# Kernel optimization log

Measured on AMD Instinct MI355X. Metric: run time of the kernel, lower is better.

Reference implementation:

```python
import jax, jax.numpy as jnp
import numpy as np

D_MODEL, D_K, D_V = 1024, 64, 64
B, S = 4, 4096


def setup_inputs() -> dict:
    key = jax.random.key(0)
    ks = jax.random.split(key, 13)
    s = 1.0 / np.sqrt(D_MODEL)
    inp = {
        "q": jax.random.normal(ks[0], (B, S, D_MODEL), jnp.float32),
        "k": jax.random.normal(ks[1], (B, S, D_MODEL), jnp.float32),
        "v": jax.random.normal(ks[2], (B, S, D_MODEL), jnp.float32),
        "mask": jax.random.randint(ks[3], (1, S, S), 0, 2, jnp.int32),
        "Wq": jax.random.normal(ks[4], (D_K, D_MODEL), jnp.float32) * s,
        "bq": jax.random.normal(ks[5], (D_K,), jnp.float32) * s,
        "Wk": jax.random.normal(ks[6], (D_K, D_MODEL), jnp.float32) * s,
        "bk": jax.random.normal(ks[7], (D_K,), jnp.float32) * s,
        "Wv": jax.random.normal(ks[8], (D_V, D_MODEL), jnp.float32) * s,
        "bv": jax.random.normal(ks[9], (D_V,), jnp.float32) * s,
        "Wo": jax.random.normal(ks[10], (D_MODEL, D_V), jnp.float32) / np.sqrt(D_V),
        "bo": jax.random.normal(ks[11], (D_MODEL,), jnp.float32) / np.sqrt(D_V),
    }
    return inp


def reference(q, k, v, mask, Wq, bq, Wk, bk, Wv, bv, Wo, bo):
    # linear projections (torch Linear: x @ W.T + b)
    qh = jnp.einsum("bsd,kd->bsk", q, Wq) + bq   # [B,S,d_k]
    kh = jnp.einsum("bsd,kd->bsk", k, Wk) + bk   # [B,S,d_k]
    vh = jnp.einsum("bsd,vd->bsv", v, Wv) + bv   # [B,S,d_v]
    scale = 1.0 / jnp.sqrt(jnp.float32(D_K))
    scores = jnp.einsum("bqk,bmk->bqm", qh, kh) * scale  # [B,S,S]
    scores = jnp.where(mask == 0, jnp.float32(-1e9), scores)
    attn = jax.nn.softmax(scores, axis=-1)
    out = jnp.einsum("bqm,bmv->bqv", attn, vh)   # [B,S,d_v]
    return jnp.einsum("bqv,dv->bqd", out, Wo) + bo
```

## Files before the change

kernel.cpp:

```cpp
#include <hip/hip_runtime.h>
#include <cmath>

typedef __attribute__((ext_vector_type(8))) short bf16x8;
typedef __attribute__((ext_vector_type(4))) short bf16x4;
typedef __attribute__((ext_vector_type(4))) float f32x4;
typedef unsigned int u32;
typedef __attribute__((address_space(1))) const u32 gu32;
typedef __attribute__((address_space(3))) u32 lu32;

constexpr int B_ = 4;
constexpr int S_ = 4096;
constexpr int DM_ = 1024;
constexpr int DK_ = 64;
constexpr int NROW = B_ * S_;

__device__ __forceinline__ short f2bf(float x) {
  union { float f; unsigned u; } c; c.f = x;
  unsigned r = (c.u + 0x7FFF + ((c.u >> 16) & 1)) >> 16;
  return (short)r;
}
__device__ __forceinline__ float bf2f(short h) {
  union { float f; unsigned u; } c; c.u = ((unsigned)(unsigned short)h) << 16;
  return c.f;
}
__device__ __forceinline__ void gl16(const void* g, void* l) {
  __builtin_amdgcn_global_load_lds((gu32*)g, (lu32*)l, 16, 0, 0);
}

__global__ __launch_bounds__(256) void prep(
    const int* __restrict__ mask, unsigned long long* __restrict__ bits,
    const float* __restrict__ Wq, const float* __restrict__ Wk,
    const float* __restrict__ Wv, short* __restrict__ wbf) {
  if (blockIdx.x < 1024) {
    const int wid = (blockIdx.x * 256 + threadIdx.x) >> 6;
    const int lane = threadIdx.x & 63;
    const size_t base = (size_t)wid * 4096;
    for (int it = 0; it < 64; ++it) {
      int m = mask[base + it * 64 + lane];
      unsigned long long b = __ballot(m != 0);
      if (lane == 0) bits[(size_t)wid * 64 + it] = b;
    }
  } else {
    const int mat = blockIdx.x - 1024;
    const float* W = mat == 0 ? Wq : (mat == 1 ? Wk : Wv);
    short* dst = wbf + (size_t)mat * DK_ * DM_;
    const int t = threadIdx.x;
#pragma unroll 4
    for (int i = 0; i < 32; ++i) {
      int idx = i * 2048 + t * 8;
      f32x4 a0 = *(const f32x4*)(W + idx);
      f32x4 a1 = *(const f32x4*)(W + idx + 4);
      bf16x8 h;
#pragma unroll
      for (int j = 0; j < 4; ++j) { h[j] = f2bf(a0[j]); h[j + 4] = f2bf(a1[j]); }
      *(bf16x8*)(dst + idx) = h;
    }
  }
}

__global__ __launch_bounds__(256, 3) void proj_mfma(
    const float* __restrict__ q, const float* __restrict__ k,
    const float* __restrict__ v, const short* __restrict__ wbf,
    const float* __restrict__ bq, const float* __restrict__ bk,
    const float* __restrict__ bv,
    short* __restrict__ qh, short* __restrict__ kh, short* __restrict__ vhT) {
  __shared__ short wlds[2][64][64];

  const int mat = blockIdx.z;
  const float* X    = mat == 0 ? q : (mat == 1 ? k : v);
  const short* W    = wbf + (size_t)mat * DK_ * DM_;
  const float* bias = mat == 0 ? bq : (mat == 1 ? bk : bv);

  const int t = threadIdx.x;
  const int row0 = blockIdx.x * 64;
  const int lane = t & 63, w = t >> 6, quad = lane >> 4, l16 = lane & 15;

  const int myrow = row0 + 16 * w + l16;
  const float* xp = X + (size_t)myrow * DM_ + quad * 8;

  const int grA = 16 * w + (lane >> 3);
  const int scolh = (((lane & 7) ^ (lane >> 3)) * 8);
  const short* wsrcA = W + (size_t)grA * DM_ + scolh;
  const short* wsrcB = W + (size_t)(grA + 8) * DM_ + scolh;
  short* wdstA0 = &wlds[0][16 * w][0] + lane * 8;
  short* wdstB0 = &wlds[0][16 * w + 8][0] + lane * 8;
  short* wdstA1 = &wlds[1][16 * w][0] + lane * 8;
  short* wdstB1 = &wlds[1][16 * w + 8][0] + lane * 8;

  const int rsw = (l16 & 7) << 4;

  f32x4 acc[4] = {};
  f32x4 xr[4][4];

  gl16(wsrcA, wdstA0);
  gl16(wsrcB, wdstB0);
#pragma unroll
  for (int pb = 0; pb < 2; ++pb) {
    const float* s = xp + pb * 64;
    xr[pb][0] = *(const f32x4*)(s + 0);
    xr[pb][1] = *(const f32x4*)(s + 4);
    xr[pb][2] = *(const f32x4*)(s + 32);
    xr[pb][3] = *(const f32x4*)(s + 36);
  }
  asm volatile("s_waitcnt vmcnt(8)" ::: "memory");
  __builtin_amdgcn_s_barrier();
  __builtin_amdgcn_sched_barrier(0);

  auto compute_step = [&](int i, int buf) {
    const char* wb = (const char*)&wlds[buf][0][0];
    bf16x8 wf[2][4];
#pragma unroll
    for (int c = 0; c < 2; ++c)
#pragma unroll
      for (int ct = 0; ct < 4; ++ct)
        wf[c][ct] = *(const bf16x8*)(wb + (16 * ct + l16) * 128 +
                                     ((c * 64 + quad * 16) ^ rsw));
#pragma unroll
    for (int c = 0; c < 2; ++c) {
      f32x4 x0 = xr[i & 3][2 * c + 0];
      f32x4 x1 = xr[i & 3][2 * c + 1];
      bf16x8 ahi, alo;
#pragma unroll
      for (int j = 0; j < 4; ++j) {
        short h0 = f2bf(x0[j]); ahi[j] = h0;     alo[j]     = f2bf(x0[j] - bf2f(h0));
        short h1 = f2bf(x1[j]); ahi[j + 4] = h1; alo[j + 4] = f2bf(x1[j] - bf2f(h1));
      }
#pragma unroll
      for (int ct = 0; ct < 4; ++ct) {
        acc[ct] = __builtin_amdgcn_mfma_f32_16x16x32_bf16(ahi, wf[c][ct], acc[ct], 0, 0, 0);
        acc[ct] = __builtin_amdgcn_mfma_f32_16x16x32_bf16(alo, wf[c][ct], acc[ct], 0, 0, 0);
      }
    }
  };

#pragma unroll 4
  for (int i = 0; i < 12; ++i) {
    const int nb = (i + 1) & 1;
    gl16(wsrcA + (i + 1) * 64, nb ? wdstA1 : wdstA0);
    gl16(wsrcB + (i + 1) * 64, nb ? wdstB1 : wdstB0);
    {
      const float* s = xp + (i + 2) * 64;
      xr[(i + 2) & 3][0] = *(const f32x4*)(s + 0);
      xr[(i + 2) & 3][1] = *(const f32x4*)(s + 4);
      xr[(i + 2) & 3][2] = *(const f32x4*)(s + 32);
      xr[(i + 2) & 3][3] = *(const f32x4*)(s + 36);
    }
    compute_step(i, i & 1);
    asm volatile("s_waitcnt vmcnt(4)" ::: "memory");
    __builtin_amdgcn_s_barrier();
    __builtin_amdgcn_sched_barrier(0);
  }

  gl16(wsrcA + 13 * 64, wdstA1);
  gl16(wsrcB + 13 * 64, wdstB1);
  {
    const float* s = xp + 14 * 64;
    xr[2][0] = *(const f32x4*)(s + 0);  xr[2][1] = *(const f32x4*)(s + 4);
    xr[2][2] = *(const f32x4*)(s + 32); xr[2][3] = *(const f32x4*)(s + 36);
  }
  compute_step(12, 0);
  asm volatile("s_waitcnt vmcnt(4)" ::: "memory");
  __builtin_amdgcn_s_barrier();
  __builtin_amdgcn_sched_barrier(0);
  gl16(wsrcA + 14 * 64, wdstA0);
  gl16(wsrcB + 14 * 64, wdstB0);
  {
    const float* s = xp + 15 * 64;
    xr[3][0] = *(const f32x4*)(s + 0);  xr[3][1] = *(const f32x4*)(s + 4);
    xr[3][2] = *(const f32x4*)(s + 32); xr[3][3] = *(const f32x4*)(s + 36);
  }
  compute_step(13, 1);
  asm volatile("s_waitcnt vmcnt(4)" ::: "memory");
  __builtin_amdgcn_s_barrier();
  __builtin_amdgcn_sched_barrier(0);
  gl16(wsrcA + 15 * 64, wdstA1);
  gl16(wsrcB + 15 * 64, wdstB1);
  compute_step(14, 0);
  asm volatile("s_waitcnt vmcnt(0)" ::: "memory");
  __builtin_amdgcn_s_barrier();
  __builtin_amdgcn_sched_barrier(0);
  compute_step(15, 1);

  float bs[4];
#pragma unroll
  for (int ct = 0; ct < 4; ++ct) bs[ct] = bias[16 * ct + l16];

  short* dstq = (mat == 0) ? qh : kh;
#pragma unroll
  for (int ct = 0; ct < 4; ++ct)
#pragma unroll
    for (int reg = 0; reg < 4; ++reg) {
      int r = row0 + 16 * w + quad * 4 + reg;
      int c = 16 * ct + l16;
      short hv = f2bf(acc[ct][reg] + bs[ct]);
      if (mat == 2)
        vhT[((size_t)(r >> 12) * DK_ + c) * S_ + (r & 4095)] = hv;
      else
        dstq[(size_t)r * DK_ + c] = hv;
    }
}

__global__ __launch_bounds__(256) void attn_mfma(
    const short* __restrict__ qh, const short* __restrict__ kh,
    const short* __restrict__ vhT, const unsigned int* __restrict__ mbits,
    float* __restrict__ Opart, float* __restrict__ mpart,
    float* __restrict__ lpart, int ns) {
  __shared__ short ks[64][72];
  __shared__ short vt[64][72];
  __shared__ short ps[4][16][72];

  const int b = blockIdx.z;
  const int split = blockIdx.y;
  const int q0 = blockIdx.x * 64;
  const int t = threadIdx.x, lane = t & 63, w = t >> 6;
  const int quad = lane >> 4, l16 = lane & 15;
  const int myq = q0 + 16 * w + l16;

  const int kt0 = split * (S_ / ns);
  const int kt1 = kt0 + S_ / ns;

  bf16x8 qf[2];
  {
    const short* src = qh + ((size_t)b * S_ + myq) * DK_ + quad * 8;
    qf[0] = *(const bf16x8*)src;
    qf[1] = *(const bf16x8*)(src + 32);
  }

  f32x4 ao[4] = {};
  float m_i = -INFINITY, l_i = 0.0f;

  const int sr = t >> 2;
  const int sseg = t & 3;

  for (int kt = kt0; kt < kt1; kt += 64) {
    __syncthreads();
    {
      const short* srck = kh + ((size_t)b * S_ + kt + sr) * DK_;
      *(bf16x8*)&ks[sr][8 * sseg]       = *(const bf16x8*)(srck + 8 * sseg);
      *(bf16x8*)&ks[sr][8 * (sseg + 4)] = *(const bf16x8*)(srck + 8 * (sseg + 4));
      const short* srcv = vhT + ((size_t)b * DK_ + sr) * S_ + kt;
      *(bf16x8*)&vt[sr][8 * sseg]       = *(const bf16x8*)(srcv + 8 * sseg);
      *(bf16x8*)&vt[sr][8 * (sseg + 4)] = *(const bf16x8*)(srcv + 8 * (sseg + 4));
    }
    const uint2 mw = *(const uint2*)&mbits[(size_t)myq * 128 + (kt >> 5)];
    __syncthreads();

    f32x4 sacc[4] = {};
#pragma unroll
    for (int c = 0; c < 2; ++c)
#pragma unroll
      for (int tt = 0; tt < 4; ++tt) {
        bf16x8 a = *(const bf16x8*)&ks[16 * tt + l16][c * 32 + quad * 8];
        sacc[tt] = __builtin_amdgcn_mfma_f32_16x16x32_bf16(a, qf[c], sacc[tt], 0, 0, 0);
      }

    float sc[16];
#pragma unroll
    for (int tt = 0; tt < 4; ++tt) {
      unsigned wrd = (tt & 2) ? mw.y : mw.x;
      int base = (tt & 1) * 16 + quad * 4;
#pragma unroll
      for (int r = 0; r < 4; ++r)
        sc[tt * 4 + r] = ((wrd >> (base + r)) & 1) ? sacc[tt][r] * 0.125f : -1e9f;
    }

    float mx = sc[0];
#pragma unroll
    for (int i = 1; i < 16; ++i) mx = fmaxf(mx, sc[i]);
    mx = fmaxf(mx, __shfl_xor(mx, 16));
    mx = fmaxf(mx, __shfl_xor(mx, 32));
    float m_new = fmaxf(m_i, mx);
    float alpha = __expf(m_i - m_new);
    float p[16], sum = 0.0f;
#pragma unroll
    for (int i = 0; i < 16; ++i) { p[i] = __expf(sc[i] - m_new); sum += p[i]; }
    sum += __shfl_xor(sum, 16);
    sum += __shfl_xor(sum, 32);
    l_i = l_i * alpha + sum;
    m_i = m_new;

#pragma unroll
    for (int tt = 0; tt < 4; ++tt) {
      bf16x4 pk;
#pragma unroll
      for (int r = 0; r < 4; ++r) pk[r] = f2bf(p[tt * 4 + r]);
      *(bf16x4*)&ps[w][l16][16 * tt + quad * 4] = pk;
    }

#pragma unroll
    for (int dt = 0; dt < 4; ++dt)
#pragma unroll
      for (int r = 0; r < 4; ++r) ao[dt][r] *= alpha;

#pragma unroll
    for (int c = 0; c < 2; ++c) {
      bf16x8 bp = *(const bf16x8*)&ps[w][l16][c * 32 + quad * 8];
#pragma unroll
      for (int dt = 0; dt < 4; ++dt) {
        bf16x8 av = *(const bf16x8*)&vt[16 * dt + l16][c * 32 + quad * 8];
        ao[dt] = __builtin_amdgcn_mfma_f32_16x16x32_bf16(av, bp, ao[dt], 0, 0, 0);
      }
    }
  }

  const size_t prow = (size_t)split * NROW + (size_t)b * S_ + myq;
#pragma unroll
  for (int dt = 0; dt < 4; ++dt)
    *(f32x4*)&Opart[prow * DK_ + 16 * dt + quad * 4] = ao[dt];
  if (quad == 0) {
    mpart[prow] = m_i;
    lpart[prow] = l_i;
  }
}

__global__ __launch_bounds__(256) void attn_combine(
    const float* __restrict__ Opart, const float* __restrict__ mpart,
    const float* __restrict__ lpart, short* __restrict__ o_bf, int ns) {
  const int t = threadIdx.x;
  const int row = blockIdx.x * 64 + (t >> 2);
  const int c0 = (t & 3) * 16;

  float M = -INFINITY;
  for (int s = 0; s < ns; ++s) M = fmaxf(M, mpart[(size_t)s * NROW + row]);
  float L = 0.0f, wt[4];
  for (int s = 0; s < ns; ++s) {
    wt[s] = __expf(mpart[(size_t)s * NROW + row] - M);
    L += wt[s] * lpart[(size_t)s * NROW + row];
  }
  float acc[16] = {};
  for (int s = 0; s < ns; ++s) {
    const float* src = Opart + ((size_t)s * NROW + row) * DK_ + c0;
#pragma unroll
    for (int j = 0; j < 16; j += 4) {
      f32x4 vv = *(const f32x4*)(src + j);
#pragma unroll
      for (int r = 0; r < 4; ++r) acc[j + r] += wt[s] * vv[r];
    }
  }
  const float inv = 1.0f / L;
  bf16x8 o0, o1;
#pragma unroll
  for (int j = 0; j < 8; ++j) {
    o0[j] = f2bf(acc[j] * inv);
    o1[j] = f2bf(acc[j + 8] * inv);
  }
  *(bf16x8*)&o_bf[(size_t)row * DK_ + c0]     = o0;
  *(bf16x8*)&o_bf[(size_t)row * DK_ + c0 + 8] = o1;
}

__global__ __launch_bounds__(256) void outproj_mfma(
    const short* __restrict__ o_bf, const float* __restrict__ Wo,
    const float* __restrict__ bo, float* __restrict__ out) {
  __shared__ short os[64][72];
  __shared__ short wos[256][72];

  const int t = threadIdx.x, lane = t & 63, w = t >> 6;
  const int quad = lane >> 4, l16 = lane & 15;
  const int s0 = blockIdx.y * 64;
  const int dm0 = blockIdx.x * 256;

  {
    int r = t >> 2, cq = (t & 3) * 16;
    const short* src = o_bf + (size_t)(s0 + r) * DK_ + cq;
    *(bf16x8*)&os[r][cq]     = *(const bf16x8*)src;
    *(bf16x8*)&os[r][cq + 8] = *(const bf16x8*)(src + 8);
  }
#pragma unroll
  for (int pass = 0; pass < 4; ++pass) {
    int r = pass * 64 + (t >> 2), cq = (t & 3) * 16;
    const float* src = Wo + (size_t)(dm0 + r) * DK_ + cq;
    f32x4 a0 = *(const f32x4*)src, a1 = *(const f32x4*)(src + 4);
    f32x4 a2 = *(const f32x4*)(src + 8), a3 = *(const f32x4*)(src + 12);
    bf16x8 v0, v1;
#pragma unroll
    for (int j = 0; j < 4; ++j) {
      v0[j] = f2bf(a0[j]); v0[j + 4] = f2bf(a1[j]);
      v1[j] = f2bf(a2[j]); v1[j + 4] = f2bf(a3[j]);
    }
    *(bf16x8*)&wos[r][cq]     = v0;
    *(bf16x8*)&wos[r][cq + 8] = v1;
  }
  __syncthreads();

  bf16x8 af[2];
#pragma unroll
  for (int c = 0; c < 2; ++c)
    af[c] = *(const bf16x8*)&os[16 * w + l16][c * 32 + quad * 8];

  f32x4 acc[16] = {};
#pragma unroll
  for (int c = 0; c < 2; ++c)
#pragma unroll
    for (int nt = 0; nt < 16; ++nt) {
      bf16x8 bw = *(const bf16x8*)&wos[16 * nt + l16][c * 32 + quad * 8];
      acc[nt] = __builtin_amdgcn_mfma_f32_16x16x32_bf16(af[c], bw, acc[nt], 0, 0, 0);
    }

  float bias_r[16];
#pragma unroll
  for (int nt = 0; nt < 16; ++nt) bias_r[nt] = bo[dm0 + 16 * nt + l16];

#pragma unroll
  for (int nt = 0; nt < 16; ++nt)
#pragma unroll
    for (int reg = 0; reg < 4; ++reg) {
      int s = s0 + 16 * w + quad * 4 + reg;
      int dm = dm0 + 16 * nt + l16;
      out[(size_t)s * DM_ + dm] = acc[nt][reg] + bias_r[nt];
    }
}

extern "C" void kernel_launch(void* const* d_in, const int* in_sizes, int n_in,
                              void* d_out, int out_size, void* d_ws,
                              size_t ws_size, hipStream_t stream) {
  (void)in_sizes; (void)n_in; (void)out_size;
  const float* q  = (const float*)d_in[0];
  const float* k  = (const float*)d_in[1];
  const float* v  = (const float*)d_in[2];
  const int* mask = (const int*)d_in[3];
  const float* Wq = (const float*)d_in[4];
  const float* bq = (const float*)d_in[5];
  const float* Wk = (const float*)d_in[6];
  const float* bk = (const float*)d_in[7];
  const float* Wv = (const float*)d_in[8];
  const float* bv = (const float*)d_in[9];
  const float* Wo = (const float*)d_in[10];
  const float* bo = (const float*)d_in[11];
  float* out = (float*)d_out;

  short* qh  = (short*)d_ws;
  short* kh  = qh + (size_t)NROW * DK_;
  short* vhT = kh + (size_t)NROW * DK_;
  unsigned int* mbits = (unsigned int*)(vhT + (size_t)NROW * DK_);
  short* o_bf = (short*)(mbits + (size_t)S_ * 128);
  float* mpart = (float*)(o_bf + (size_t)NROW * DK_);
  float* lpart = mpart + 4 * NROW;
  float* Opart = lpart + 4 * NROW;
  short* wbf = (short*)Opart;

  const size_t base_bytes = (size_t)((char*)Opart - (char*)d_ws);
  const size_t per_split = (size_t)NROW * DK_ * sizeof(float);
  int ns = 1;
  if (ws_size >= base_bytes + 4 * per_split) ns = 4;
  else if (ws_size >= base_bytes + 2 * per_split) ns = 2;

  prep<<<1027, 256, 0, stream>>>(mask, (unsigned long long*)mbits,
                                 Wq, Wk, Wv, wbf);
  proj_mfma<<<dim3(NROW / 64, 1, 3), 256, 0, stream>>>(
      q, k, v, wbf, bq, bk, bv, qh, kh, vhT);
  attn_mfma<<<dim3(S_ / 64, ns, B_), 256, 0, stream>>>(
      qh, kh, vhT, mbits, Opart, mpart, lpart, ns);
  attn_combine<<<NROW / 64, 256, 0, stream>>>(Opart, mpart, lpart, o_bf, ns);
  outproj_mfma<<<dim3(DM_ / 256, NROW / 64), 256, 0, stream>>>(o_bf, Wo, bo, out);
}
```

Baseline: 373.0 us.

## Double-buffer K/V tiles via async global-to-LDS loads and pre-convert Wo

The attention kernel now stages K and V tiles straight into LDS with global_load_lds into a double buffer using an XOR swizzle. The next tile and its mask words are prefetched while the current tile is computed, which replaces two barriers per step with one waitcnt plus one barrier. This is meant to hide global load latency behind MFMA and softmax work. Separately, Wo is converted to bf16 once in the prep kernel, so the many outproj blocks no longer each reconvert fp32 weights. The cost is more LDS use and manual wait and barrier handling that could cause races if miscounted.

Result: slower. 384.1 us (+3.0%).

```diff
diff --git a/kernel.cpp b/kernel.cpp
--- a/kernel.cpp
+++ b/kernel.cpp
@@ -30,7 +30,8 @@
 __global__ __launch_bounds__(256) void prep(
     const int* __restrict__ mask, unsigned long long* __restrict__ bits,
     const float* __restrict__ Wq, const float* __restrict__ Wk,
-    const float* __restrict__ Wv, short* __restrict__ wbf) {
+    const float* __restrict__ Wv, const float* __restrict__ Wo,
+    short* __restrict__ wbf, short* __restrict__ wobf) {
   if (blockIdx.x < 1024) {
     const int wid = (blockIdx.x * 256 + threadIdx.x) >> 6;
     const int lane = threadIdx.x & 63;
@@ -42,8 +43,8 @@
     }
   } else {
     const int mat = blockIdx.x - 1024;
-    const float* W = mat == 0 ? Wq : (mat == 1 ? Wk : Wv);
-    short* dst = wbf + (size_t)mat * DK_ * DM_;
+    const float* W = mat == 0 ? Wq : (mat == 1 ? Wk : (mat == 2 ? Wv : Wo));
+    short* dst = (mat < 3) ? (wbf + (size_t)mat * DK_ * DM_) : wobf;
     const int t = threadIdx.x;
 #pragma unroll 4
     for (int i = 0; i < 32; ++i) {
@@ -205,8 +206,7 @@
     const short* __restrict__ vhT, const unsigned int* __restrict__ mbits,
     float* __restrict__ Opart, float* __restrict__ mpart,
     float* __restrict__ lpart, int ns) {
-  __shared__ short ks[64][72];
-  __shared__ short vt[64][72];
+  __shared__ short kvs[2][2][64][64];
   __shared__ short ps[4][16][72];
 
   const int b = blockIdx.z;
@@ -216,8 +216,8 @@
   const int quad = lane >> 4, l16 = lane & 15;
   const int myq = q0 + 16 * w + l16;
 
+  const int nst = (S_ / ns) / 64;
   const int kt0 = split * (S_ / ns);
-  const int kt1 = kt0 + S_ / ns;
 
   bf16x8 qf[2];
   {
@@ -226,38 +226,64 @@
     qf[1] = *(const bf16x8*)(src + 32);
   }
 
+  const int srow = 16 * w + (lane >> 3);
+  const int scolh = ((lane & 7) ^ (lane >> 3)) * 8;
+  const short* ksrcA = kh + ((size_t)b * S_ + kt0 + srow) * DK_ + scolh;
+  const short* ksrcB = kh + ((size_t)b * S_ + kt0 + srow + 8) * DK_ + scolh;
+  const short* vsrcA = vhT + ((size_t)b * DK_ + srow) * S_ + kt0 + scolh;
+  const short* vsrcB = vhT + ((size_t)b * DK_ + srow + 8) * S_ + kt0 + scolh;
+  short* kd0 = &kvs[0][0][16 * w][0] + lane * 8;
+  short* kd1 = &kvs[1][0][16 * w][0] + lane * 8;
+  short* vd0 = &kvs[0][1][16 * w][0] + lane * 8;
+  short* vd1 = &kvs[1][1][16 * w][0] + lane * 8;
+
+  auto stage = [&](int buf, int i) {
+    const size_t ko = (size_t)i * 64 * DK_;
+    const size_t vo = (size_t)i * 64;
+    gl16(ksrcA + ko, buf ? kd1 : kd0);
+    gl16(ksrcB + ko, (buf ? kd1 : kd0) + 512);
+    gl16(vsrcA + vo, buf ? vd1 : vd0);
+    gl16(vsrcB + vo, (buf ? vd1 : vd0) + 512);
+  };
+
+  const int rswz = (l16 & 7) << 4;
+
   f32x4 ao[4] = {};
   float m_i = -INFINITY, l_i = 0.0f;
 
-  const int sr = t >> 2;
-  const int sseg = t & 3;
-
-  for (int kt = kt0; kt < kt1; kt += 64) {
-    __syncthreads();
-    {
-      const short* srck = kh + ((size_t)b * S_ + kt + sr) * DK_;
-      *(bf16x8*)&ks[sr][8 * sseg]       = *(const bf16x8*)(srck + 8 * sseg);
-      *(bf16x8*)&ks[sr][8 * (sseg + 4)] = *(const bf16x8*)(srck + 8 * (sseg + 4));
-      const short* srcv = vhT + ((size_t)b * DK_ + sr) * S_ + kt;
-      *(bf16x8*)&vt[sr][8 * sseg]       = *(const bf16x8*)(srcv + 8 * sseg);
-      *(bf16x8*)&vt[sr][8 * (sseg + 4)] = *(const bf16x8*)(srcv + 8 * (sseg + 4));
-    }
-    const uint2 mw = *(const uint2*)&mbits[(size_t)myq * 128 + (kt >> 5)];
-    __syncthreads();
+  stage(0, 0);
+  uint2 mw_c = *(const uint2*)&mbits[(size_t)myq * 128 + (kt0 >> 5)];
+  asm volatile("s_waitcnt vmcnt(0)" ::: "memory");
+  __builtin_amdgcn_s_barrier();
+  __builtin_amdgcn_sched_barrier(0);
+
+  int buf = 0;
+#pragma unroll 1
+  for (int i = 0; i < nst; ++i) {
+    uint2 mw_n = mw_c;
+    if (i + 1 < nst) {
+      stage(buf ^ 1, i + 1);
+      mw_n = *(const uint2*)&mbits[(size_t)myq * 128 +
+                                   ((kt0 + (i + 1) * 64) >> 5)];
+    }
+
+    const char* kb = (const char*)&kvs[buf][0][0][0];
+    const char* vb = (const char*)&kvs[buf][1][0][0];
 
     f32x4 sacc[4] = {};
 #pragma unroll
     for (int c = 0; c < 2; ++c)
 #pragma unroll
       for (int tt = 0; tt < 4; ++tt) {
-        bf16x8 a = *(const bf16x8*)&ks[16 * tt + l16][c * 32 + quad * 8];
+        bf16x8 a = *(const bf16x8*)(kb + (16 * tt + l16) * 128 +
+                                    ((c * 64 + quad * 16) ^ rswz));
         sacc[tt] = __builtin_amdgcn_mfma_f32_16x16x32_bf16(a, qf[c], sacc[tt], 0, 0, 0);
       }
 
     float sc[16];
 #pragma unroll
     for (int tt = 0; tt < 4; ++tt) {
-      unsigned wrd = (tt & 2) ? mw.y : mw.x;
+      unsigned wrd = (tt & 2) ? mw_c.y : mw_c.x;
       int base = (tt & 1) * 16 + quad * 4;
 #pragma unroll
       for (int r = 0; r < 4; ++r)
@@ -266,14 +292,14 @@
 
     float mx = sc[0];
 #pragma unroll
-    for (int i = 1; i < 16; ++i) mx = fmaxf(mx, sc[i]);
+    for (int i2 = 1; i2 < 16; ++i2) mx = fmaxf(mx, sc[i2]);
     mx = fmaxf(mx, __shfl_xor(mx, 16));
     mx = fmaxf(mx, __shfl_xor(mx, 32));
     float m_new = fmaxf(m_i, mx);
     float alpha = __expf(m_i - m_new);
     float p[16], sum = 0.0f;
 #pragma unroll
-    for (int i = 0; i < 16; ++i) { p[i] = __expf(sc[i] - m_new); sum += p[i]; }
+    for (int i2 = 0; i2 < 16; ++i2) { p[i2] = __expf(sc[i2] - m_new); sum += p[i2]; }
     sum += __shfl_xor(sum, 16);
     sum += __shfl_xor(sum, 32);
     l_i = l_i * alpha + sum;
@@ -297,10 +323,17 @@
       bf16x8 bp = *(const bf16x8*)&ps[w][l16][c * 32 + quad * 8];
 #pragma unroll
       for (int dt = 0; dt < 4; ++dt) {
-        bf16x8 av = *(const bf16x8*)&vt[16 * dt + l16][c * 32 + quad * 8];
+        bf16x8 av = *(const bf16x8*)(vb + (16 * dt + l16) * 128 +
+                                     ((c * 64 + quad * 16) ^ rswz));
         ao[dt] = __builtin_amdgcn_mfma_f32_16x16x32_bf16(av, bp, ao[dt], 0, 0, 0);
       }
     }
+
+    asm volatile("s_waitcnt vmcnt(0)" ::: "memory");
+    __builtin_amdgcn_s_barrier();
+    __builtin_amdgcn_sched_barrier(0);
+    buf ^= 1;
+    mw_c = mw_n;
   }
 
   const size_t prow = (size_t)split * NROW + (size_t)b * S_ + myq;
@@ -349,7 +382,7 @@
 }
 
 __global__ __launch_bounds__(256) void outproj_mfma(
-    const short* __restrict__ o_bf, const float* __restrict__ Wo,
+    const short* __restrict__ o_bf, const short* __restrict__ wobf,
     const float* __restrict__ bo, float* __restrict__ out) {
   __shared__ short os[64][72];
   __shared__ short wos[256][72];
@@ -368,17 +401,9 @@
 #pragma unroll
   for (int pass = 0; pass < 4; ++pass) {
     int r = pass * 64 + (t >> 2), cq = (t & 3) * 16;
-    const float* src = Wo + (size_t)(dm0 + r) * DK_ + cq;
-    f32x4 a0 = *(const f32x4*)src, a1 = *(const f32x4*)(src + 4);
-    f32x4 a2 = *(const f32x4*)(src + 8), a3 = *(const f32x4*)(src + 12);
-    bf16x8 v0, v1;
-#pragma unroll
-    for (int j = 0; j < 4; ++j) {
-      v0[j] = f2bf(a0[j]); v0[j + 4] = f2bf(a1[j]);
-      v1[j] = f2bf(a2[j]); v1[j + 4] = f2bf(a3[j]);
-    }
-    *(bf16x8*)&wos[r][cq]     = v0;
-    *(bf16x8*)&wos[r][cq + 8] = v1;
+    const short* src = wobf + (size_t)(dm0 + r) * DK_ + cq;
+    *(bf16x8*)&wos[r][cq]     = *(const bf16x8*)src;
+    *(bf16x8*)&wos[r][cq + 8] = *(const bf16x8*)(src + 8);
   }
   __syncthreads();
 
@@ -435,7 +460,8 @@
   short* o_bf = (short*)(mbits + (size_t)S_ * 128);
   float* mpart = (float*)(o_bf + (size_t)NROW * DK_);
   float* lpart = mpart + 4 * NROW;
-  float* Opart = lpart + 4 * NROW;
+  short* wobf = (short*)(lpart + 4 * NROW);
+  float* Opart = (float*)(wobf + (size_t)DM_ * DK_);
   short* wbf = (short*)Opart;
 
   const size_t base_bytes = (size_t)((char*)Opart - (char*)d_ws);
@@ -444,12 +470,12 @@
   if (ws_size >= base_bytes + 4 * per_split) ns = 4;
   else if (ws_size >= base_bytes + 2 * per_split) ns = 2;
 
-  prep<<<1027, 256, 0, stream>>>(mask, (unsigned long long*)mbits,
-                                 Wq, Wk, Wv, wbf);
+  prep<<<1028, 256, 0, stream>>>(mask, (unsigned long long*)mbits,
+                                 Wq, Wk, Wv, Wo, wbf, wobf);
   proj_mfma<<<dim3(NROW / 64, 1, 3), 256, 0, stream>>>(
       q, k, v, wbf, bq, bk, bv, qh, kh, vhT);
   attn_mfma<<<dim3(S_ / 64, ns, B_), 256, 0, stream>>>(
       qh, kh, vhT, mbits, Opart, mpart, lpart, ns);
   attn_combine<<<NROW / 64, 256, 0, stream>>>(Opart, mpart, lpart, o_bf, ns);
-  outproj_mfma<<<dim3(DM_ / 256, NROW / 64), 256, 0, stream>>>(o_bf, Wo, bo, out);
-}
+  outproj_mfma<<<dim3(DM_ / 256, NROW / 64), 256, 0, stream>>>(o_bf, wobf, bo, out);
+}
```
